# Performance work log

Measured on AMD Instinct MI355X. Metric: run time of the kernel, lower is better.

The kernel has to match this reference:

```python
import jax, jax.numpy as jnp
import numpy as np


def _shared_mlp(x, W, s, b):
    # 1x1 conv over channel dim (last axis) + folded BN (scale/shift) + ReLU
    # x: (..., Cin), W: (Cout, Cin), s/b: (Cout,)
    return jax.nn.relu(jnp.einsum('...c,oc->...o', x, W) * s + b)


def setup_inputs() -> dict:
    key = jax.random.key(0)
    ks = jax.random.split(key, 15)
    B, N, K, C = 4, 4096, 32, 64
    D1, D2, DH = 64, 64, 128
    sc = 0.1
    return {
        'xyz': jax.random.normal(ks[0], (B, N, 3), dtype=jnp.float32),
        'features': jax.random.normal(ks[1], (B, C, N), dtype=jnp.float32),
        'idx': jax.random.randint(ks[2], (N, K), 0, N, dtype=jnp.int32),
        'W_gu': jax.random.normal(ks[3], (D1, 6), dtype=jnp.float32) * sc,
        's_gu': jnp.ones((D1,), jnp.float32),
        'b_gu': jax.random.normal(ks[4], (D1,), dtype=jnp.float32) * sc,
        'W_gv': jax.random.normal(ks[5], (D2, C), dtype=jnp.float32) * sc,
        's_gv': jnp.ones((D2,), jnp.float32),
        'b_gv': jax.random.normal(ks[6], (D2,), dtype=jnp.float32) * sc,
        'W_h': jax.random.normal(ks[7], (DH, D1 + D2), dtype=jnp.float32) * sc,
        's_h': jnp.ones((DH,), jnp.float32),
        'b_h': jax.random.normal(ks[8], (DH,), dtype=jnp.float32) * sc,
        'W_f': jax.random.normal(ks[9], (C, DH), dtype=jnp.float32) * sc,
        's_f': jnp.ones((C,), jnp.float32),
        'b_f': jax.random.normal(ks[10], (C,), dtype=jnp.float32) * sc,
    }


def reference(xyz, features, idx, W_gu, s_gu, b_gu, W_gv, s_gv, b_gv,
              W_h, s_h, b_h, W_f, s_f, b_f):
    # xyz: (B,N,3), features: (B,C,N), idx: (N,K) neighbor indices per point
    feats = jnp.swapaxes(features, 1, 2)              # (B,N,C)
    xyz_nb = xyz[:, idx, :]                           # (B,N,K,3) random gather
    feat_nb = feats[:, idx, :]                        # (B,N,K,C)
    K = idx.shape[1]
    center_xyz = jnp.broadcast_to(xyz[:, :, None, :], xyz_nb.shape)
    rel_xyz = jnp.concatenate([center_xyz, xyz_nb], axis=-1)   # (B,N,K,6)
    rel_feat = feat_nb + feats[:, :, None, :]                  # (B,N,K,C)

    gu = _shared_mlp(rel_xyz, W_gu, s_gu, b_gu)       # (B,N,K,D1)
    gv = _shared_mlp(rel_feat, W_gv, s_gv, b_gv)      # (B,N,K,D2)
    fuse = jnp.concatenate([gu, gv], axis=-1)         # (B,N,K,D1+D2)
    h = _shared_mlp(fuse, W_h, s_h, b_h)              # (B,N,K,DH)
    pooled = jnp.mean(h, axis=2)                      # (B,N,DH) mean over K
    out = _shared_mlp(pooled, W_f, s_f, b_f)          # (B,N,C)
    out = jnp.swapaxes(out, 1, 2) + features          # (B,C,N) residual
    return (xyz, out)
```

## Files before the change

kernel.cpp:

```cpp
#include <hip/hip_runtime.h>

#define B_  4
#define N_  4096
#define K_  32
#define C_  64
#define DH_ 128
#define PPW 8

typedef _Float16 half2v __attribute__((ext_vector_type(2)));
typedef _Float16 half8  __attribute__((ext_vector_type(8)));
typedef __fp16   fp16x2 __attribute__((ext_vector_type(2)));
typedef float  floatx16 __attribute__((ext_vector_type(16)));
typedef unsigned int uint_t;

union HU { half2v h; uint_t u; };
union HU2 { fp16x2 h; uint_t u; };

__device__ __forceinline__ uint_t pk2(float a, float b) {
    HU2 x; x.h = __builtin_amdgcn_cvt_pkrtz(a, b);
    return x.u;
}

__global__ __launch_bounds__(256) void k_prep(
    const float* __restrict__ xyz,
    const float* __restrict__ features,
    const float* __restrict__ W_gv,
    const float* __restrict__ W_gu,
    const float* __restrict__ s_gu, const float* __restrict__ b_gu,
    const float* __restrict__ s_gv, const float* __restrict__ b_gv,
    const float* __restrict__ W_h,  const float* __restrict__ s_h,
    float* __restrict__ out_xyz,
    _Float16* __restrict__ Bpack,
    uint_t* __restrict__ QsH,
    uint_t* __restrict__ PcatH)
{
    const int blk = blockIdx.x;
    const int b   = blk >> 8;
    const int n0  = (blk & 255) * 16;
    const int t   = threadIdx.x;

    if (t < 48) { int e = blk*48 + t; out_xyz[e] = xyz[e]; }
    if (t >= 64 && t < 80) {
        int e = blk*16 + (t - 64);
        int j = e & 7, l = (e >> 3) & 63, c = (e >> 9) & 7, ob = e >> 12;
        int o = ob*32 + (l & 31);
        int i = c*16 + (l >> 5)*8 + j;
        Bpack[e] = (_Float16)(W_h[o*DH_ + i] * s_h[o]);
    }

    __shared__ __align__(16) float ftile[64 * 17];
    __shared__ __align__(16) float wtile[64 * 68];

    {
        const int c = t >> 2, nq = t & 3;
        const float4 f4 = *(const float4*)&features[(b*C_ + c)*N_ + n0 + nq*4];
        ftile[c*17 + nq*4 + 0] = f4.x;
        ftile[c*17 + nq*4 + 1] = f4.y;
        ftile[c*17 + nq*4 + 2] = f4.z;
        ftile[c*17 + nq*4 + 3] = f4.w;
    }
#pragma unroll
    for (int r = 0; r < 4; r++) {
        const int e4 = r*256 + t, o = e4 >> 4, c0 = (e4 & 15)*4;
        const float4 w4 = *(const float4*)&W_gv[o*C_ + c0];
        wtile[(c0+0)*68 + o] = w4.x;
        wtile[(c0+1)*68 + o] = w4.y;
        wtile[(c0+2)*68 + o] = w4.z;
        wtile[(c0+3)*68 + o] = w4.w;
    }
    __syncthreads();

    const int n  = t >> 4;
    const int oq = t & 15;
    const int o0 = oq * 4;

    float acc[4] = {};
#pragma unroll 4
    for (int c = 0; c < 64; c++) {
        const float a = ftile[c*17 + n];
        const float4 wv = *(const float4*)&wtile[c*68 + o0];
        acc[0] = fmaf(a, wv.x, acc[0]);
        acc[1] = fmaf(a, wv.y, acc[1]);
        acc[2] = fmaf(a, wv.z, acc[2]);
        acc[3] = fmaf(a, wv.w, acc[3]);
    }

    const int bn = b*N_ + n0 + n;
    const float x0 = xyz[bn*3+0], x1 = xyz[bn*3+1], x2 = xyz[bn*3+2];

    const float4 sgu = *(const float4*)&s_gu[o0];
    const float4 bgu = *(const float4*)&b_gu[o0];
    const float4 sgv = *(const float4*)&s_gv[o0];
    const float4 bgv = *(const float4*)&b_gv[o0];

    float q[4], r[4];
#pragma unroll
    for (int jj = 0; jj < 4; jj++) {
        const int o = o0 + jj;
        q[jj] = x0*W_gu[o*6+0] + x1*W_gu[o*6+1] + x2*W_gu[o*6+2];
        r[jj] = x0*W_gu[o*6+3] + x1*W_gu[o*6+4] + x2*W_gu[o*6+5];
    }
    uint2 qa, pa;
    qa.x = pk2(q[0]*sgu.x+bgu.x, q[1]*sgu.y+bgu.y);
    qa.y = pk2(q[2]*sgu.z+bgu.z, q[3]*sgu.w+bgu.w);
    pa.x = pk2(r[0]*sgu.x, r[1]*sgu.y);
    pa.y = pk2(r[2]*sgu.z, r[3]*sgu.w);
    *(uint2*)&QsH  [bn*64 + oq*2] = qa;
    *(uint2*)&PcatH[bn*64 + oq*2] = pa;
    qa.x = pk2(acc[0]*sgv.x+bgv.x, acc[1]*sgv.y+bgv.y);
    qa.y = pk2(acc[2]*sgv.z+bgv.z, acc[3]*sgv.w+bgv.w);
    pa.x = pk2(acc[0]*sgv.x, acc[1]*sgv.y);
    pa.y = pk2(acc[2]*sgv.z, acc[3]*sgv.w);
    *(uint2*)&QsH  [bn*64 + 32 + oq*2] = qa;
    *(uint2*)&PcatH[bn*64 + 32 + oq*2] = pa;
}

__global__ __launch_bounds__(128) void k_main(
    const int*      __restrict__ idx,
    const uint_t*   __restrict__ QsH,
    const uint_t*   __restrict__ PcatH,
    const _Float16* __restrict__ Bpack,
    const float*    __restrict__ b_h,
    const float*    __restrict__ W_f,
    const float*    __restrict__ s_f, const float* __restrict__ b_f,
    const float*    __restrict__ features,
    float* __restrict__ outF)
{
    const int t    = threadIdx.x;
    const int ohu  = __builtin_amdgcn_readfirstlane(t >> 6);
    const int lane = t & 63;
    const int m    = lane & 31;
    const int hh   = lane >> 5;

    __shared__ uint_t fuse[2][32 * 66];
    __shared__ __align__(16) float pooled[PPW * 132];

    half8 Bf[2][8];
#pragma unroll
    for (int ob = 0; ob < 2; ob++)
#pragma unroll
        for (int c = 0; c < 8; c++)
            Bf[ob][c] = *(const half8*)&Bpack[(((ohu*2 + ob)*8 + c)*64 + lane)*8];

    const float bh0 = b_h[(ohu*2+0)*32 + m];
    const float bh1 = b_h[(ohu*2+1)*32 + m];

    const int bnb   = blockIdx.x * PPW;
    const int base0 = bnb & ~(N_ - 1);
    const half2v zero2 = {(_Float16)0.f, (_Float16)0.f};

    uint_t pg[16];
    uint_t qw;
    int js[16];

    {
        const int n0p = bnb & (N_ - 1);
        const int* ip = idx + n0p*K_ + ohu*16;
#pragma unroll
        for (int it = 0; it < 16; it++) js[it] = ip[it];
        qw = QsH[(size_t)bnb*64 + lane];
#pragma unroll
        for (int it = 0; it < 16; it++)
            pg[it] = PcatH[((size_t)(base0 + js[it]) << 6) + lane];
#pragma unroll
        for (int it = 0; it < 16; it++) {
            HU a, pval; a.u = qw; pval.u = pg[it];
            half2v v = a.h + pval.h;
            v = __builtin_elementwise_max(v, zero2);
            HU o2; o2.h = v;
            fuse[0][(ohu*16 + it)*66 + lane] = o2.u;
        }
    }
    __syncthreads();

#pragma unroll
    for (int p = 0; p < PPW; p++) {
        const int cur = p & 1, nxt = cur ^ 1;

        uint_t qw_n = 0;
        if (p + 1 < PPW) {
            const int np = (bnb + p + 1) & (N_ - 1);
            const int* ip = idx + np*K_ + ohu*16;
#pragma unroll
            for (int it = 0; it < 16; it++) js[it] = ip[it];
            qw_n = QsH[(size_t)(bnb + p + 1)*64 + lane];
#pragma unroll
            for (int it = 0; it < 16; it++)
                pg[it] = PcatH[((size_t)(base0 + js[it]) << 6) + lane];
        }

        floatx16 acc0 = {}, acc1 = {};
#pragma unroll
        for (int c = 0; c < 8; c++) {
            const int wb = m*66 + c*8 + hh*4;
            union { uint_t u[4]; half8 h; } av;
            *(uint2*)&av.u[0] = *(const uint2*)&fuse[cur][wb];
            *(uint2*)&av.u[2] = *(const uint2*)&fuse[cur][wb + 2];
            acc0 = __builtin_amdgcn_mfma_f32_32x32x16_f16(av.h, Bf[0][c], acc0, 0, 0, 0);
            acc1 = __builtin_amdgcn_mfma_f32_32x32x16_f16(av.h, Bf[1][c], acc1, 0, 0, 0);
        }
        float v0 = 0.f, v1 = 0.f;
#pragma unroll
        for (int rg = 0; rg < 16; rg++) {
            v0 += fmaxf(acc0[rg] + bh0, 0.f);
            v1 += fmaxf(acc1[rg] + bh1, 0.f);
        }
        v0 += __shfl_xor(v0, 32);
        v1 += __shfl_xor(v1, 32);
        if (hh == 0) {
            pooled[p*132 + (ohu*2+0)*32 + m] = v0;
            pooled[p*132 + (ohu*2+1)*32 + m] = v1;
        }

        if (p + 1 < PPW) {
#pragma unroll
            for (int it = 0; it < 16; it++) {
                HU a, pval; a.u = qw_n; pval.u = pg[it];
                half2v v = a.h + pval.h;
                v = __builtin_elementwise_max(v, zero2);
                HU o2; o2.h = v;
                fuse[nxt][(ohu*16 + it)*66 + lane] = o2.u;
            }
        }
        __syncthreads();
    }

    const int b   = bnb >> 12;
    const int n0  = bnb & (N_ - 1);
    const int c   = t >> 1;
    const int r2  = t & 1;

    float acc[4] = {};
#pragma unroll 4
    for (int i0 = 0; i0 < DH_; i0 += 4) {
        const float4 wv = *(const float4*)&W_f[c*DH_ + i0];
#pragma unroll
        for (int r = 0; r < 4; r++) {
            const float4 p4 = *(const float4*)&pooled[(r2*4 + r)*132 + i0];
            acc[r] += wv.x*p4.x + wv.y*p4.y + wv.z*p4.z + wv.w*p4.w;
        }
    }
    const float sfc = s_f[c] * (1.f/(float)K_);
    const float bfc = b_f[c];
    const float4 fr = *(const float4*)&features[(b*C_ + c)*N_ + n0 + r2*4];
    float4 ov;
    ov.x = fmaxf(acc[0]*sfc + bfc, 0.f) + fr.x;
    ov.y = fmaxf(acc[1]*sfc + bfc, 0.f) + fr.y;
    ov.z = fmaxf(acc[2]*sfc + bfc, 0.f) + fr.z;
    ov.w = fmaxf(acc[3]*sfc + bfc, 0.f) + fr.w;
    *(float4*)&outF[(b*C_ + c)*N_ + n0 + r2*4] = ov;
}

extern "C" void kernel_launch(void* const* d_in, const int* in_sizes, int n_in,
                              void* d_out, int out_size, void* d_ws, size_t ws_size,
                              hipStream_t stream)
{
    const float* xyz      = (const float*)d_in[0];
    const float* features = (const float*)d_in[1];
    const int*   idx      = (const int*)  d_in[2];
    const float* W_gu     = (const float*)d_in[3];
    const float* s_gu     = (const float*)d_in[4];
    const float* b_gu     = (const float*)d_in[5];
    const float* W_gv     = (const float*)d_in[6];
    const float* s_gv     = (const float*)d_in[7];
    const float* b_gv     = (const float*)d_in[8];
    const float* W_h      = (const float*)d_in[9];
    const float* s_h      = (const float*)d_in[10];
    const float* b_h      = (const float*)d_in[11];
    const float* W_f      = (const float*)d_in[12];
    const float* s_f      = (const float*)d_in[13];
    const float* b_f      = (const float*)d_in[14];

    float* out  = (float*)d_out;
    float* outF = out + B_*N_*3;

    char* wp = (char*)d_ws;
    uint_t*   QsH   = (uint_t*)wp;   wp += (size_t)B_*N_*64*4;
    uint_t*   PcatH = (uint_t*)wp;   wp += (size_t)B_*N_*64*4;
    _Float16* Bpack = (_Float16*)wp; wp += DH_*DH_*2;

    k_prep<<<B_*(N_/16), 256, 0, stream>>>(xyz, features, W_gv, W_gu,
                                           s_gu, b_gu, s_gv, b_gv, W_h, s_h,
                                           out, Bpack, QsH, PcatH);
    k_main<<<(B_*N_)/PPW, 128, 0, stream>>>(idx, QsH, PcatH, Bpack, b_h,
                                            W_f, s_f, b_f, features, outF);
}
```

Baseline: 129.5 us.

## Use single-wave blocks computing all output columns, dropping barriers

k_main now runs one 64-lane wave per block. That wave owns all 128 output columns (four MFMA accumulators) and gathers all 32 neighbours itself, so the double-buffered LDS and the __syncthreads calls go away. Points per block drop from 8 to 4. The bias add is folded into the ReLU as max(acc, -b) plus 32*b after the sum. The aim is to remove barrier stalls and the cross-wave split. The cost is much higher register pressure (64 B-fragment registers, 32 gathered values, 64 accumulators), which may lower occupancy or cause spills.

```diff
diff --git a/kernel.cpp b/kernel.cpp
--- a/kernel.cpp
+++ b/kernel.cpp
@@ -5,7 +5,7 @@
 #define K_  32
 #define C_  64
 #define DH_ 128
-#define PPW 8
+#define PPW 4
 
 typedef _Float16 half2v __attribute__((ext_vector_type(2)));
 typedef _Float16 half8  __attribute__((ext_vector_type(8)));
@@ -115,7 +115,7 @@
     *(uint2*)&PcatH[bn*64 + 32 + oq*2] = pa;
 }
 
-__global__ __launch_bounds__(128) void k_main(
+__global__ __launch_bounds__(64, 2) void k_main(
     const int*      __restrict__ idx,
     const uint_t*   __restrict__ QsH,
     const uint_t*   __restrict__ PcatH,
@@ -126,129 +126,138 @@
     const float*    __restrict__ features,
     float* __restrict__ outF)
 {
-    const int t    = threadIdx.x;
-    const int ohu  = __builtin_amdgcn_readfirstlane(t >> 6);
-    const int lane = t & 63;
+    const int lane = threadIdx.x;
     const int m    = lane & 31;
     const int hh   = lane >> 5;
 
-    __shared__ uint_t fuse[2][32 * 66];
+    __shared__ uint_t fuse[32 * 66];
     __shared__ __align__(16) float pooled[PPW * 132];
 
-    half8 Bf[2][8];
-#pragma unroll
-    for (int ob = 0; ob < 2; ob++)
+    half8 Bf[4][8];
+#pragma unroll
+    for (int ob = 0; ob < 4; ob++)
 #pragma unroll
         for (int c = 0; c < 8; c++)
-            Bf[ob][c] = *(const half8*)&Bpack[(((ohu*2 + ob)*8 + c)*64 + lane)*8];
-
-    const float bh0 = b_h[(ohu*2+0)*32 + m];
-    const float bh1 = b_h[(ohu*2+1)*32 + m];
+            Bf[ob][c] = *(const half8*)&Bpack[((ob*8 + c)*64 + lane)*8];
+
+    float nbh[4], b32[4];
+#pragma unroll
+    for (int ob = 0; ob < 4; ob++) {
+        const float bh = b_h[ob*32 + m];
+        nbh[ob] = -bh;
+        b32[ob] = 32.f * bh;
+    }
 
     const int bnb   = blockIdx.x * PPW;
     const int base0 = bnb & ~(N_ - 1);
     const half2v zero2 = {(_Float16)0.f, (_Float16)0.f};
-
-    uint_t pg[16];
+    (void)zero2;
+
+    uint_t pg[32];
     uint_t qw;
-    int js[16];
 
     {
         const int n0p = bnb & (N_ - 1);
-        const int* ip = idx + n0p*K_ + ohu*16;
-#pragma unroll
-        for (int it = 0; it < 16; it++) js[it] = ip[it];
+        const int* ip = idx + n0p*K_;
+        int js[32];
+#pragma unroll
+        for (int it = 0; it < 32; it++) js[it] = ip[it];
         qw = QsH[(size_t)bnb*64 + lane];
 #pragma unroll
-        for (int it = 0; it < 16; it++)
+        for (int it = 0; it < 32; it++)
             pg[it] = PcatH[((size_t)(base0 + js[it]) << 6) + lane];
 #pragma unroll
-        for (int it = 0; it < 16; it++) {
-            HU a, pval; a.u = qw; pval.u = pg[it];
-            half2v v = a.h + pval.h;
-            v = __builtin_elementwise_max(v, zero2);
-            HU o2; o2.h = v;
-            fuse[0][(ohu*16 + it)*66 + lane] = o2.u;
-        }
-    }
-    __syncthreads();
+        for (int it = 0; it < 32; it++) {
+            HU a, pv; a.u = qw; pv.u = pg[it];
+            half2v v = a.h + pv.h;
+            HU o2; o2.h = __builtin_elementwise_max(v, (half2v){(_Float16)0.f,(_Float16)0.f});
+            fuse[it*66 + lane] = o2.u;
+        }
+    }
 
 #pragma unroll
     for (int p = 0; p < PPW; p++) {
-        const int cur = p & 1, nxt = cur ^ 1;
-
         uint_t qw_n = 0;
         if (p + 1 < PPW) {
             const int np = (bnb + p + 1) & (N_ - 1);
-            const int* ip = idx + np*K_ + ohu*16;
-#pragma unroll
-            for (int it = 0; it < 16; it++) js[it] = ip[it];
+            const int* ip = idx + np*K_;
+            int js[32];
+#pragma unroll
+            for (int it = 0; it < 32; it++) js[it] = ip[it];
             qw_n = QsH[(size_t)(bnb + p + 1)*64 + lane];
 #pragma unroll
-            for (int it = 0; it < 16; it++)
+            for (int it = 0; it < 32; it++)
                 pg[it] = PcatH[((size_t)(base0 + js[it]) << 6) + lane];
         }
 
-        floatx16 acc0 = {}, acc1 = {};
+        floatx16 acc0 = {}, acc1 = {}, acc2 = {}, acc3 = {};
 #pragma unroll
         for (int c = 0; c < 8; c++) {
             const int wb = m*66 + c*8 + hh*4;
             union { uint_t u[4]; half8 h; } av;
-            *(uint2*)&av.u[0] = *(const uint2*)&fuse[cur][wb];
-            *(uint2*)&av.u[2] = *(const uint2*)&fuse[cur][wb + 2];
+            *(uint2*)&av.u[0] = *(const uint2*)&fuse[wb];
+            *(uint2*)&av.u[2] = *(const uint2*)&fuse[wb + 2];
             acc0 = __builtin_amdgcn_mfma_f32_32x32x16_f16(av.h, Bf[0][c], acc0, 0, 0, 0);
             acc1 = __builtin_amdgcn_mfma_f32_32x32x16_f16(av.h, Bf[1][c], acc1, 0, 0, 0);
-        }
-        float v0 = 0.f, v1 = 0.f;
+            acc2 = __builtin_amdgcn_mfma_f32_32x32x16_f16(av.h, Bf[2][c], acc2, 0, 0, 0);
+            acc3 = __builtin_amdgcn_mfma_f32_32x32x16_f16(av.h, Bf[3][c], acc3, 0, 0, 0);
+        }
+
+        float v0 = 0.f, v1 = 0.f, v2 = 0.f, v3 = 0.f;
 #pragma unroll
         for (int rg = 0; rg < 16; rg++) {
-            v0 += fmaxf(acc0[rg] + bh0, 0.f);
-            v1 += fmaxf(acc1[rg] + bh1, 0.f);
+            v0 += fmaxf(acc0[rg], nbh[0]);
+            v1 += fmaxf(acc1[rg], nbh[1]);
+            v2 += fmaxf(acc2[rg], nbh[2]);
+            v3 += fmaxf(acc3[rg], nbh[3]);
         }
         v0 += __shfl_xor(v0, 32);
         v1 += __shfl_xor(v1, 32);
+        v2 += __shfl_xor(v2, 32);
+        v3 += __shfl_xor(v3, 32);
         if (hh == 0) {
-            pooled[p*132 + (ohu*2+0)*32 + m] = v0;
-            pooled[p*132 + (ohu*2+1)*32 + m] = v1;
+            pooled[p*132 +  0 + m] = v0 + b32[0];
+            pooled[p*132 + 32 + m] = v1 + b32[1];
+            pooled[p*132 + 64 + m] = v2 + b32[2];
+            pooled[p*132 + 96 + m] = v3 + b32[3];
         }
 
         if (p + 1 < PPW) {
 #pragma unroll
-            for (int it = 0; it < 16; it++) {
-                HU a, pval; a.u = qw_n; pval.u = pg[it];
-                half2v v = a.h + pval.h;
-                v = __builtin_elementwise_max(v, zero2);
-                HU o2; o2.h = v;
-                fuse[nxt][(ohu*16 + it)*66 + lane] = o2.u;
+            for (int it = 0; it < 32; it++) {
+                HU a, pv; a.u = qw_n; pv.u = pg[it];
+                half2v v = a.h + pv.h;
+                HU o2; o2.h = __builtin_elementwise_max(v, (half2v){(_Float16)0.f,(_Float16)0.f});
+                fuse[it*66 + lane] = o2.u;
             }
         }
-        __syncthreads();
-    }
-
-    const int b   = bnb >> 12;
-    const int n0  = bnb & (N_ - 1);
-    const int c   = t >> 1;
-    const int r2  = t & 1;
-
-    float acc[4] = {};
-#pragma unroll 4
+    }
+
+    const int b  = bnb >> 12;
+    const int n0 = bnb & (N_ - 1);
+    const int c  = lane;
+
+    float wreg[DH_ / 4][4];
+    float accf[PPW] = {};
+#pragma unroll 8
     for (int i0 = 0; i0 < DH_; i0 += 4) {
         const float4 wv = *(const float4*)&W_f[c*DH_ + i0];
-#pragma unroll
-        for (int r = 0; r < 4; r++) {
-            const float4 p4 = *(const float4*)&pooled[(r2*4 + r)*132 + i0];
-            acc[r] += wv.x*p4.x + wv.y*p4.y + wv.z*p4.z + wv.w*p4.w;
+        (void)wreg;
+#pragma unroll
+        for (int r = 0; r < PPW; r++) {
+            const float4 p4 = *(const float4*)&pooled[r*132 + i0];
+            accf[r] += wv.x*p4.x + wv.y*p4.y + wv.z*p4.z + wv.w*p4.w;
         }
     }
     const float sfc = s_f[c] * (1.f/(float)K_);
     const float bfc = b_f[c];
-    const float4 fr = *(const float4*)&features[(b*C_ + c)*N_ + n0 + r2*4];
+    const float4 fr = *(const float4*)&features[(b*C_ + c)*N_ + n0];
     float4 ov;
-    ov.x = fmaxf(acc[0]*sfc + bfc, 0.f) + fr.x;
-    ov.y = fmaxf(acc[1]*sfc + bfc, 0.f) + fr.y;
-    ov.z = fmaxf(acc[2]*sfc + bfc, 0.f) + fr.z;
-    ov.w = fmaxf(acc[3]*sfc + bfc, 0.f) + fr.w;
-    *(float4*)&outF[(b*C_ + c)*N_ + n0 + r2*4] = ov;
+    ov.x = fmaxf(accf[0]*sfc + bfc, 0.f) + fr.x;
+    ov.y = fmaxf(accf[1]*sfc + bfc, 0.f) + fr.y;
+    ov.z = fmaxf(accf[2]*sfc + bfc, 0.f) + fr.z;
+    ov.w = fmaxf(accf[3]*sfc + bfc, 0.f) + fr.w;
+    *(float4*)&outF[(b*C_ + c)*N_ + n0] = ov;
 }
 
 extern "C" void kernel_launch(void* const* d_in, const int* in_sizes, int n_in,
@@ -282,6 +291,6 @@
     k_prep<<<B_*(N_/16), 256, 0, stream>>>(xyz, features, W_gv, W_gu,
                                            s_gu, b_gu, s_gv, b_gv, W_h, s_h,
                                            out, Bpack, QsH, PcatH);
-    k_main<<<(B_*N_)/PPW, 128, 0, stream>>>(idx, QsH, PcatH, Bpack, b_h,
-                                            W_f, s_f, b_f, features, outF);
-}
+    k_main<<<(B_*N_)/PPW, 64, 0, stream>>>(idx, QsH, PcatH, Bpack, b_h,
+                                           W_f, s_f, b_f, features, outF);
+}
```

Result: no change. 130.4 us (+0.7%).

## Split final MLP epilogue out of main kernel into separate post kernel

Applied to the files above, without the earlier changes.

The main kernel no longer runs the W_f projection, BN and residual epilogue. It writes pooled sums to a global workspace, and a new k_post kernel does the 128->64 projection using shared-memory tiles of pooled rows and a transposed W_f, then writes coalesced output. The bias-plus-ReLU inside the pooling is also rewritten as max(acc, -b) with 32*b added afterwards, which saves one add per element. In exchange there is an extra kernel launch and an 8 MB global round trip for Pool, while k_main gets smaller shared memory and fewer registers, so occupancy may rise.

```diff
diff --git a/kernel.cpp b/kernel.cpp
--- a/kernel.cpp
+++ b/kernel.cpp
@@ -121,10 +121,7 @@
     const uint_t*   __restrict__ PcatH,
     const _Float16* __restrict__ Bpack,
     const float*    __restrict__ b_h,
-    const float*    __restrict__ W_f,
-    const float*    __restrict__ s_f, const float* __restrict__ b_f,
-    const float*    __restrict__ features,
-    float* __restrict__ outF)
+    float* __restrict__ Pool)
 {
     const int t    = threadIdx.x;
     const int ohu  = __builtin_amdgcn_readfirstlane(t >> 6);
@@ -133,7 +130,6 @@
     const int hh   = lane >> 5;
 
     __shared__ uint_t fuse[2][32 * 66];
-    __shared__ __align__(16) float pooled[PPW * 132];
 
     half8 Bf[2][8];
 #pragma unroll
@@ -142,12 +138,13 @@
         for (int c = 0; c < 8; c++)
             Bf[ob][c] = *(const half8*)&Bpack[(((ohu*2 + ob)*8 + c)*64 + lane)*8];
 
-    const float bh0 = b_h[(ohu*2+0)*32 + m];
-    const float bh1 = b_h[(ohu*2+1)*32 + m];
+    const float bh0  = b_h[(ohu*2+0)*32 + m];
+    const float bh1  = b_h[(ohu*2+1)*32 + m];
+    const float nbh0 = -bh0, nbh1 = -bh1;
+    const float b32_0 = 32.f * bh0, b32_1 = 32.f * bh1;
 
     const int bnb   = blockIdx.x * PPW;
     const int base0 = bnb & ~(N_ - 1);
-    const half2v zero2 = {(_Float16)0.f, (_Float16)0.f};
 
     uint_t pg[16];
     uint_t qw;
@@ -166,8 +163,7 @@
         for (int it = 0; it < 16; it++) {
             HU a, pval; a.u = qw; pval.u = pg[it];
             half2v v = a.h + pval.h;
-            v = __builtin_elementwise_max(v, zero2);
-            HU o2; o2.h = v;
+            HU o2; o2.h = __builtin_elementwise_max(v, (half2v){(_Float16)0.f,(_Float16)0.f});
             fuse[0][(ohu*16 + it)*66 + lane] = o2.u;
         }
     }
@@ -202,14 +198,14 @@
         float v0 = 0.f, v1 = 0.f;
 #pragma unroll
         for (int rg = 0; rg < 16; rg++) {
-            v0 += fmaxf(acc0[rg] + bh0, 0.f);
-            v1 += fmaxf(acc1[rg] + bh1, 0.f);
+            v0 += fmaxf(acc0[rg], nbh0);
+            v1 += fmaxf(acc1[rg], nbh1);
         }
         v0 += __shfl_xor(v0, 32);
         v1 += __shfl_xor(v1, 32);
         if (hh == 0) {
-            pooled[p*132 + (ohu*2+0)*32 + m] = v0;
-            pooled[p*132 + (ohu*2+1)*32 + m] = v1;
+            Pool[(size_t)(bnb + p)*128 + (ohu*2+0)*32 + m] = v0 + b32_0;
+            Pool[(size_t)(bnb + p)*128 + (ohu*2+1)*32 + m] = v1 + b32_1;
         }
 
         if (p + 1 < PPW) {
@@ -217,38 +213,73 @@
             for (int it = 0; it < 16; it++) {
                 HU a, pval; a.u = qw_n; pval.u = pg[it];
                 half2v v = a.h + pval.h;
-                v = __builtin_elementwise_max(v, zero2);
-                HU o2; o2.h = v;
+                HU o2; o2.h = __builtin_elementwise_max(v, (half2v){(_Float16)0.f,(_Float16)0.f});
                 fuse[nxt][(ohu*16 + it)*66 + lane] = o2.u;
             }
         }
         __syncthreads();
     }
-
-    const int b   = bnb >> 12;
-    const int n0  = bnb & (N_ - 1);
-    const int c   = t >> 1;
-    const int r2  = t & 1;
+}
+
+__global__ __launch_bounds__(256) void k_post(
+    const float* __restrict__ Pool,
+    const float* __restrict__ W_f,
+    const float* __restrict__ s_f, const float* __restrict__ b_f,
+    const float* __restrict__ features,
+    float* __restrict__ outF)
+{
+    const int b   = blockIdx.x >> 8;
+    const int n0  = (blockIdx.x & 255) * 16;
+    const int t   = threadIdx.x;
+    const int bn0 = b*N_ + n0;
+
+    __shared__ __align__(16) float pt[16 * 132];
+    __shared__ __align__(16) float wt[128 * 68];
+    __shared__ float ot[64 * 17];
+
+    for (int e = t; e < 16*128; e += 256) {
+        const int nl = e >> 7, i = e & 127;
+        pt[nl*132 + i] = Pool[(size_t)(bn0 + nl)*128 + i];
+    }
+    for (int e = t; e < C_*DH_; e += 256) {
+        const int c = e >> 7, i = e & 127;
+        wt[i*68 + c] = W_f[e];
+    }
+    __syncthreads();
+
+    const int nl = t >> 4;
+    const int cq = t & 15;
+    const int c0 = cq * 4;
 
     float acc[4] = {};
 #pragma unroll 4
-    for (int i0 = 0; i0 < DH_; i0 += 4) {
-        const float4 wv = *(const float4*)&W_f[c*DH_ + i0];
-#pragma unroll
-        for (int r = 0; r < 4; r++) {
-            const float4 p4 = *(const float4*)&pooled[(r2*4 + r)*132 + i0];
-            acc[r] += wv.x*p4.x + wv.y*p4.y + wv.z*p4.z + wv.w*p4.w;
-        }
-    }
-    const float sfc = s_f[c] * (1.f/(float)K_);
-    const float bfc = b_f[c];
-    const float4 fr = *(const float4*)&features[(b*C_ + c)*N_ + n0 + r2*4];
-    float4 ov;
-    ov.x = fmaxf(acc[0]*sfc + bfc, 0.f) + fr.x;
-    ov.y = fmaxf(acc[1]*sfc + bfc, 0.f) + fr.y;
-    ov.z = fmaxf(acc[2]*sfc + bfc, 0.f) + fr.z;
-    ov.w = fmaxf(acc[3]*sfc + bfc, 0.f) + fr.w;
-    *(float4*)&outF[(b*C_ + c)*N_ + n0 + r2*4] = ov;
+    for (int i = 0; i < DH_; i++) {
+        const float p = pt[nl*132 + i];
+        const float4 wv = *(const float4*)&wt[i*68 + c0];
+        acc[0] = fmaf(p, wv.x, acc[0]);
+        acc[1] = fmaf(p, wv.y, acc[1]);
+        acc[2] = fmaf(p, wv.z, acc[2]);
+        acc[3] = fmaf(p, wv.w, acc[3]);
+    }
+    const float4 sf = *(const float4*)&s_f[c0];
+    const float4 bf = *(const float4*)&b_f[c0];
+    const float inv_k = 1.f / (float)K_;
+    ot[(c0+0)*17 + nl] = fmaxf(acc[0]*inv_k*sf.x + bf.x, 0.f);
+    ot[(c0+1)*17 + nl] = fmaxf(acc[1]*inv_k*sf.y + bf.y, 0.f);
+    ot[(c0+2)*17 + nl] = fmaxf(acc[2]*inv_k*sf.z + bf.z, 0.f);
+    ot[(c0+3)*17 + nl] = fmaxf(acc[3]*inv_k*sf.w + bf.w, 0.f);
+    __syncthreads();
+
+    {
+        const int c = t >> 2, nq = t & 3;
+        const float4 fr = *(const float4*)&features[(b*C_ + c)*N_ + n0 + nq*4];
+        float4 ov;
+        ov.x = ot[c*17 + nq*4 + 0] + fr.x;
+        ov.y = ot[c*17 + nq*4 + 1] + fr.y;
+        ov.z = ot[c*17 + nq*4 + 2] + fr.z;
+        ov.w = ot[c*17 + nq*4 + 3] + fr.w;
+        *(float4*)&outF[(b*C_ + c)*N_ + n0 + nq*4] = ov;
+    }
 }
 
 extern "C" void kernel_launch(void* const* d_in, const int* in_sizes, int n_in,
@@ -277,11 +308,12 @@
     char* wp = (char*)d_ws;
     uint_t*   QsH   = (uint_t*)wp;   wp += (size_t)B_*N_*64*4;
     uint_t*   PcatH = (uint_t*)wp;   wp += (size_t)B_*N_*64*4;
+    float*    Pool  = (float*)wp;    wp += (size_t)B_*N_*128*4;
     _Float16* Bpack = (_Float16*)wp; wp += DH_*DH_*2;
 
     k_prep<<<B_*(N_/16), 256, 0, stream>>>(xyz, features, W_gv, W_gu,
                                            s_gu, b_gu, s_gv, b_gv, W_h, s_h,
                                            out, Bpack, QsH, PcatH);
-    k_main<<<(B_*N_)/PPW, 128, 0, stream>>>(idx, QsH, PcatH, Bpack, b_h,
-                                            W_f, s_f, b_f, features, outF);
-}
+    k_main<<<(B_*N_)/PPW, 128, 0, stream>>>(idx, QsH, PcatH, Bpack, b_h, Pool);
+    k_post<<<B_*(N_/16), 256, 0, stream>>>(Pool, W_f, s_f, b_f, features, outF);
+}
```

Measured after the change: 132.6 us. 2.4% more time.
